# Optimization experiments

Hardware: AMD Instinct MI355X
Metric: run time of the kernel (lower is better)

The kernel has to match this reference:

```python
import jax, jax.numpy as jnp
import numpy as np

N = 50000          # num nodes
E = 800000         # num edges
D = 128            # dim_in == embed_dim
MAX_NODES = 4      # hard-coded in SortConv.__init__
EPS = 1e-5


def setup_inputs() -> dict:
    key = jax.random.key(0)
    ks = jax.random.split(key, 16)
    inp = {
        'x': jax.random.normal(ks[0], (N, D), jnp.float32),
        'edge_index': jax.random.randint(ks[1], (2, E), 0, N, jnp.int32),
    }
    for i in range(2):
        o = 2 + 6 * i
        W = jax.random.normal(ks[o], (D, D), jnp.float32) * (2.0 / (D + D)) ** 0.5
        W = W / jnp.linalg.norm(W, axis=1, keepdims=True)   # reset_parameters row-normalization
        inp[f'W{i}'] = W
        inp[f'b{i}'] = jnp.zeros((D,), jnp.float32)
        inp[f'cw{i}'] = jax.random.normal(ks[o + 1], (MAX_NODES,), jnp.float32) * (2.0 / (MAX_NODES + 1)) ** 0.5
        inp[f'cb{i}'] = jnp.zeros((1,), jnp.float32)
        inp[f'a{i}'] = jax.random.uniform(ks[o + 2], (1,), jnp.float32, -1.0, 1.0)  # LinearCombination scalar
        inp[f'g{i}'] = jnp.ones((D,), jnp.float32)
        inp[f'be{i}'] = jnp.zeros((D,), jnp.float32)
        inp[f'blank{i}'] = jnp.zeros((D,), jnp.float32)      # learnable blank vector
    return inp


def sort_conv(x, edge_index, blank, W, b, cw, cb, a):
    n, d = x.shape
    e = edge_index.shape[1]
    src, dst = edge_index[0], edge_index[1]
    msgs = x[src]                                            # [E, D] raw messages (lin_project not applied to messages)
    order = jnp.argsort(dst)                                 # stable sort by destination (index_sort)
    dst_s = dst[order]
    counts = jax.ops.segment_sum(jnp.ones((e,), jnp.int32), dst, num_segments=n + 1)
    starts = jnp.concatenate([jnp.zeros((1,), jnp.int32), jnp.cumsum(counts)[:-1].astype(jnp.int32)])
    pos = jnp.arange(e, dtype=jnp.int32) - starts[dst_s]     # rank within each neighborhood
    slot = jnp.where(pos < MAX_NODES, pos, MAX_NODES)        # overflow edges -> trash slot (to_dense_batch truncation)
    dense = jnp.zeros((n + 1, MAX_NODES + 1, d), x.dtype).at[dst_s, slot].set(msgs[order])
    mask = jnp.zeros((n + 1, MAX_NODES + 1), bool).at[dst_s, slot].set(True)
    dense, mask = dense[:, :MAX_NODES], mask[:, :MAX_NODES]  # [N+1, 4, D], [N+1, 4]
    blank_p = W @ blank + b                                  # lin_project applied only to blank vector
    filled = dense + (~mask)[..., None].astype(x.dtype) * blank_p
    srt = jnp.sort(filled, axis=1)                           # per-feature sort over neighbor slots
    out = jnp.einsum('nmd,m->nd', srt, cw) + cb              # vector collapse: Linear(max_nodes, 1)
    node_out, blank_new = out[:-1], out[-1]                  # last row = all-blank graph -> new blank
    return a * x + node_out, a * blank + blank_new           # LinearCombination combine (num_repeats=1)


def batch_norm(h, g, be):
    mu = h.mean(0)
    var = h.var(0)
    return (h - mu) / jnp.sqrt(var + EPS) * g + be


def reference(x, edge_index, W0, b0, cw0, cb0, a0, g0, be0, blank0,
              W1, b1, cw1, cb1, a1, g1, be1, blank1):
    layers = [(W0, b0, cw0, cb0, a0, g0, be0, blank0),
              (W1, b1, cw1, cb1, a1, g1, be1, blank1)]
    for (W, b, cw, cb, a, g, be, blank) in layers:
        h, _ = sort_conv(x, edge_index, blank, W, b, cw, cb, a)
        h = batch_norm(h, g, be)
        x = x + h                                            # residual connection
    return x
```

## Files before the change

kernel.cpp:

```cpp
#include <hip/hip_runtime.h>
#include <climits>

constexpr int N_NODES = 50000;
constexpr int N_EDGES = 800000;
constexpr int DIM     = 128;
constexpr int DIM4    = DIM / 4;
constexpr float BN_EPS = 1e-5f;

constexpr int EMPTY = 0x7F7F7F7F;

constexpr int NC = 16;
constexpr int EC = 16;
constexpr int NODES_PER_NC = N_NODES / NC;
constexpr int EDGES_PER_EC = N_EDGES / EC;
constexpr int E4_PER_EC    = EDGES_PER_EC / 4;
constexpr int SEL_THREADS  = 1024;

constexpr int NODES_PER_ITER  = 8;
constexpr int CONV_ITERS      = 2;
constexpr int NODES_PER_BLOCK = NODES_PER_ITER * CONV_ITERS;
constexpr int CONV_GRID = N_NODES / NODES_PER_BLOCK;

constexpr int NBUCKETS = 64;
constexpr int NB_MERGE = (N_NODES + 255) / 256;

__device__ inline float4 f4min(float4 a, float4 b) {
    return make_float4(fminf(a.x,b.x), fminf(a.y,b.y), fminf(a.z,b.z), fminf(a.w,b.w));
}
__device__ inline float4 f4max(float4 a, float4 b) {
    return make_float4(fmaxf(a.x,b.x), fmaxf(a.y,b.y), fmaxf(a.z,b.z), fmaxf(a.w,b.w));
}
__device__ inline float4 f4add(float4 a, float4 b) {
    return make_float4(a.x+b.x, a.y+b.y, a.z+b.z, a.w+b.w);
}
__device__ inline float4 f4fma(float s, float4 v, float4 acc) {
    return make_float4(fmaf(s,v.x,acc.x), fmaf(s,v.y,acc.y), fmaf(s,v.z,acc.z), fmaf(s,v.w,acc.w));
}

__global__ __launch_bounds__(SEL_THREADS)
void select_stageA_kernel(const int* __restrict__ dst,
                          int* __restrict__ tables) {
    __shared__ int slot[NODES_PER_NC * 4];
    const int nc = blockIdx.x & (NC - 1);
    const int ec = blockIdx.x >> 4;
    const int t  = threadIdx.x;

    for (int i = t; i < NODES_PER_NC * 4; i += SEL_THREADS) slot[i] = EMPTY;
    __syncthreads();

    const int r0 = nc * NODES_PER_NC;
    const int4* __restrict__ dst4 = (const int4*)dst;
    const int base4 = ec * E4_PER_EC;
    for (int i = t; i < E4_PER_EC; i += SEL_THREADS) {
        const int4 d = dst4[base4 + i];
        const int ebase = 4 * (base4 + i);
        #define TRY_INS(comp, off) {                                        \
            unsigned n_ = (unsigned)((comp) - r0);                          \
            if (n_ < (unsigned)NODES_PER_NC) {                              \
                int cur_ = ebase + (off);                                   \
                _Pragma("unroll")                                           \
                for (int j_ = 0; j_ < 4; ++j_) {                            \
                    int old_ = atomicMin(&slot[4 * n_ + j_], cur_);         \
                    if (old_ == EMPTY) break;                               \
                    cur_ = max(cur_, old_);                                 \
                } } }
        TRY_INS(d.x, 0); TRY_INS(d.y, 1); TRY_INS(d.z, 2); TRY_INS(d.w, 3);
        #undef TRY_INS
    }
    __syncthreads();

    int4* __restrict__ out = (int4*)tables + (size_t)ec * N_NODES + r0;
    const int4* __restrict__ sl4 = (const int4*)slot;
    for (int n = t; n < NODES_PER_NC; n += SEL_THREADS) out[n] = sl4[n];
}

__global__ __launch_bounds__(256)
void select_stageB_kernel(const int* __restrict__ tables,
                          const int* __restrict__ src,
                          int4* __restrict__ srcs4,
                          float* __restrict__ stats_part,
                          const float* __restrict__ W0, const float* __restrict__ b0,
                          const float* __restrict__ bl0,
                          const float* __restrict__ W1, const float* __restrict__ b1,
                          const float* __restrict__ bl1,
                          float* __restrict__ bp) {
    const int t = threadIdx.x;

    if (blockIdx.x >= NB_MERGE) {
        if (t < DIM) {
            int l = blockIdx.x - NB_MERGE;
            const float* W  = l ? W1  : W0;
            const float* b  = l ? b1  : b0;
            const float* bl = l ? bl1 : bl0;
            float s = 0.f;
            #pragma unroll 8
            for (int j = 0; j < DIM; ++j) s += W[t * DIM + j] * bl[j];
            bp[l * DIM + t] = s + b[t];
        }
        return;
    }

    const int gid = blockIdx.x * 256 + t;
    if (gid < 2 * NBUCKETS * 256) stats_part[gid] = 0.f;

    const int v = gid;
    if (v >= N_NODES) return;

    int b0_ = EMPTY, b1_ = EMPTY, b2_ = EMPTY, b3_ = EMPTY;
    #pragma unroll
    for (int ec = 0; ec < EC; ++ec) {
        const int4 c = ((const int4*)tables)[(size_t)ec * N_NODES + v];
        if (c.x >= b3_) continue;
        #define INS(val) {                                          \
            int x_ = (val);                                         \
            if (x_ < b3_) { b3_ = x_;                               \
                int tm;                                             \
                if (b3_ < b2_) { tm = b2_; b2_ = b3_; b3_ = tm; }   \
                if (b2_ < b1_) { tm = b1_; b1_ = b2_; b2_ = tm; }   \
                if (b1_ < b0_) { tm = b0_; b0_ = b1_; b1_ = tm; } } }
        INS(c.x); INS(c.y); INS(c.z); INS(c.w);
        #undef INS
    }
    int4 o;
    o.x = (b0_ < N_EDGES) ? src[b0_] : -1;
    o.y = (b1_ < N_EDGES) ? src[b1_] : -1;
    o.z = (b2_ < N_EDGES) ? src[b2_] : -1;
    o.w = (b3_ < N_EDGES) ? src[b3_] : -1;
    srcs4[v] = o;
}

__global__ __launch_bounds__(256)
void conv_stats_kernel(const float* __restrict__ x,
                       const int4* __restrict__ srcs4,
                       const float* __restrict__ bp,
                       const float* __restrict__ cw,
                       const float* __restrict__ cb,
                       const float* __restrict__ a,
                       float* __restrict__ h,
                       float* __restrict__ stats_part) {
    const int t    = threadIdx.x;
    const int d4   = t & (DIM4 - 1);
    const int nsub = t >> 5;

    const float4* __restrict__ x4 = (const float4*)x;
    float4*       __restrict__ h4 = (float4*)h;

    const float aa = a[0];
    const float c0 = cw[0], c1 = cw[1], c2 = cw[2], c3 = cw[3];
    const float cbv = cb[0];
    const float4 bpv = ((const float4*)bp)[d4];

    const int v0 = blockIdx.x * NODES_PER_BLOCK + nsub;
    const int v1 = v0 + NODES_PER_ITER;

    const int4 s0 = srcs4[v0];
    const int4 s1 = srcs4[v1];

    float4 g00 = x4[(size_t)max(s0.x, 0) * DIM4 + d4];
    float4 g01 = x4[(size_t)max(s0.y, 0) * DIM4 + d4];
    float4 g02 = x4[(size_t)max(s0.z, 0) * DIM4 + d4];
    float4 g03 = x4[(size_t)max(s0.w, 0) * DIM4 + d4];
    float4 g10 = x4[(size_t)max(s1.x, 0) * DIM4 + d4];
    float4 g11 = x4[(size_t)max(s1.y, 0) * DIM4 + d4];
    float4 g12 = x4[(size_t)max(s1.z, 0) * DIM4 + d4];
    float4 g13 = x4[(size_t)max(s1.w, 0) * DIM4 + d4];
    float4 xv0 = x4[(size_t)v0 * DIM4 + d4];
    float4 xv1 = x4[(size_t)v1 * DIM4 + d4];

    float4 s  = make_float4(0.f, 0.f, 0.f, 0.f);
    float4 s2 = make_float4(0.f, 0.f, 0.f, 0.f);

    #define CSWAP4(p, q) { float4 lo = f4min(p, q); float4 hi = f4max(p, q); p = lo; q = hi; }
    {
        float4 m0 = (s0.x >= 0) ? g00 : bpv;
        float4 m1 = (s0.y >= 0) ? g01 : bpv;
        float4 m2 = (s0.z >= 0) ? g02 : bpv;
        float4 m3 = (s0.w >= 0) ? g03 : bpv;
        CSWAP4(m0, m1); CSWAP4(m2, m3); CSWAP4(m0, m2); CSWAP4(m1, m3); CSWAP4(m1, m2);
        float4 hv = make_float4(cbv, cbv, cbv, cbv);
        hv = f4fma(c0, m0, hv);
        hv = f4fma(c1, m1, hv);
        hv = f4fma(c2, m2, hv);
        hv = f4fma(c3, m3, hv);
        hv = f4fma(aa, xv0, hv);
        h4[(size_t)v0 * DIM4 + d4] = hv;
        s  = f4add(s, hv);
        s2 = f4add(s2, make_float4(hv.x*hv.x, hv.y*hv.y, hv.z*hv.z, hv.w*hv.w));
    }
    {
        float4 m0 = (s1.x >= 0) ? g10 : bpv;
        float4 m1 = (s1.y >= 0) ? g11 : bpv;
        float4 m2 = (s1.z >= 0) ? g12 : bpv;
        float4 m3 = (s1.w >= 0) ? g13 : bpv;
        CSWAP4(m0, m1); CSWAP4(m2, m3); CSWAP4(m0, m2); CSWAP4(m1, m3); CSWAP4(m1, m2);
        float4 hv = make_float4(cbv, cbv, cbv, cbv);
        hv = f4fma(c0, m0, hv);
        hv = f4fma(c1, m1, hv);
        hv = f4fma(c2, m2, hv);
        hv = f4fma(c3, m3, hv);
        hv = f4fma(aa, xv1, hv);
        h4[(size_t)v1 * DIM4 + d4] = hv;
        s  = f4add(s, hv);
        s2 = f4add(s2, make_float4(hv.x*hv.x, hv.y*hv.y, hv.z*hv.z, hv.w*hv.w));
    }
    #undef CSWAP4

    s.x  += __shfl_down(s.x, 32);  s.y  += __shfl_down(s.y, 32);
    s.z  += __shfl_down(s.z, 32);  s.w  += __shfl_down(s.w, 32);
    s2.x += __shfl_down(s2.x, 32); s2.y += __shfl_down(s2.y, 32);
    s2.z += __shfl_down(s2.z, 32); s2.w += __shfl_down(s2.w, 32);

    __shared__ float4 ls[4][32];
    __shared__ float4 ls2[4][32];
    const int wave = t >> 6;
    const int lane = t & 63;
    if (lane < 32) { ls[wave][lane] = s; ls2[wave][lane] = s2; }
    __syncthreads();
    if (t < 32) {
        float* bucket = stats_part + (size_t)(blockIdx.x & (NBUCKETS - 1)) * 256;
        float4 fs  = f4add(f4add(ls[0][t],  ls[1][t]),  f4add(ls[2][t],  ls[3][t]));
        float4 fs2 = f4add(f4add(ls2[0][t], ls2[1][t]), f4add(ls2[2][t], ls2[3][t]));
        atomicAdd(&bucket[4*t + 0], fs.x);
        atomicAdd(&bucket[4*t + 1], fs.y);
        atomicAdd(&bucket[4*t + 2], fs.z);
        atomicAdd(&bucket[4*t + 3], fs.w);
        atomicAdd(&bucket[DIM + 4*t + 0], fs2.x);
        atomicAdd(&bucket[DIM + 4*t + 1], fs2.y);
        atomicAdd(&bucket[DIM + 4*t + 2], fs2.z);
        atomicAdd(&bucket[DIM + 4*t + 3], fs2.w);
    }
}

__global__ void reduce_finalize_kernel(const float* __restrict__ stats_part,
                                       float* __restrict__ final) {
    __shared__ float acc[256];
    int t = threadIdx.x;
    float s = 0.f;
    #pragma unroll 8
    for (int k = 0; k < NBUCKETS; ++k) s += stats_part[k * 256 + t];
    acc[t] = s;
    __syncthreads();
    if (t < 128) {
        constexpr float invN = 1.0f / (float)N_NODES;
        float mu = acc[t] * invN;
        float iv = rsqrtf(acc[128 + t] * invN - mu * mu + BN_EPS);
        final[t]       = mu;
        final[128 + t] = iv;
    }
}

__global__ void bn_apply_kernel(const float* __restrict__ xin,
                                const float* __restrict__ h,
                                const float* __restrict__ final,
                                const float* __restrict__ g,
                                const float* __restrict__ be,
                                float* __restrict__ xout) {
    int idx = blockIdx.x * blockDim.x + threadIdx.x;
    constexpr int TOTAL4 = N_NODES * DIM4;
    if (idx >= TOTAL4) return;
    int d4 = idx & (DIM4 - 1);

    float4 mu = ((const float4*)final)[d4];
    float4 iv = ((const float4*)(final + DIM))[d4];
    float4 hv = ((const float4*)h)[idx];
    float4 xv = ((const float4*)xin)[idx];
    float4 gv = ((const float4*)g)[d4];
    float4 bv = ((const float4*)be)[d4];

    float4 o;
    o.x = xv.x + (hv.x - mu.x) * iv.x * gv.x + bv.x;
    o.y = xv.y + (hv.y - mu.y) * iv.y * gv.y + bv.y;
    o.z = xv.z + (hv.z - mu.z) * iv.z * gv.z + bv.z;
    o.w = xv.w + (hv.w - mu.w) * iv.w * gv.w + bv.w;
    ((float4*)xout)[idx] = o;
}

extern "C" void kernel_launch(void* const* d_in, const int* in_sizes, int n_in,
                              void* d_out, int out_size, void* d_ws, size_t ws_size,
                              hipStream_t stream) {
    const float* x0  = (const float*)d_in[0];
    const int*   ei  = (const int*)d_in[1];
    const int*   src = ei;
    const int*   dst = ei + N_EDGES;

    const float* W[2]; const float* b[2]; const float* cw[2]; const float* cb[2];
    const float* a[2]; const float* g[2]; const float* be[2]; const float* blank[2];
    for (int i = 0; i < 2; ++i) {
        int o = 2 + 8 * i;
        W[i]     = (const float*)d_in[o + 0];
        b[i]     = (const float*)d_in[o + 1];
        cw[i]    = (const float*)d_in[o + 2];
        cb[i]    = (const float*)d_in[o + 3];
        a[i]     = (const float*)d_in[o + 4];
        g[i]     = (const float*)d_in[o + 5];
        be[i]    = (const float*)d_in[o + 6];
        blank[i] = (const float*)d_in[o + 7];
    }

    char* ws = (char*)d_ws;
    int*   srcs       = (int*)ws;
    float* h          = (float*)(srcs + 4 * N_NODES);
    int*   tables     = (int*)h;
    float* stats_part = h + (size_t)N_NODES * DIM;
    float* final_     = stats_part + 2 * NBUCKETS * 256;
    float* bp         = final_ + 512;

    float* xout = (float*)d_out;

    select_stageA_kernel<<<NC * EC, SEL_THREADS, 0, stream>>>(dst, tables);
    select_stageB_kernel<<<NB_MERGE + 2, 256, 0, stream>>>(
        tables, src, (int4*)srcs, stats_part,
        W[0], b[0], blank[0], W[1], b[1], blank[1], bp);

    for (int l = 0; l < 2; ++l) {
        const float* xin = (l == 0) ? x0 : xout;
        float* sp = stats_part + (size_t)l * NBUCKETS * 256;
        conv_stats_kernel<<<CONV_GRID, 256, 0, stream>>>(
            xin, (const int4*)srcs, bp + l * DIM, cw[l], cb[l], a[l], h, sp);
        reduce_finalize_kernel<<<1, 256, 0, stream>>>(sp, final_ + l * 256);
        bn_apply_kernel<<<(N_NODES * DIM4 + 255) / 256, 256, 0, stream>>>(
            xin, h, final_ + l * 256, g[l], be[l], xout);
    }
}
```

Baseline: 207.9 us.

## Fuse conv, batch-norm stats and apply via a grid-wide spin barrier

The conv/stats, reduce-finalize and BN-apply kernels become one kernel per layer. Each block keeps its computed h and x values in registers for 40 nodes, adds its partial sums to the stat buckets, then waits at a grid-wide atomic-counter barrier. After the barrier it reduces the buckets and writes the normalized output directly. This drops the h write/read round trip, the second read of x and two launches per layer. It relies on all 1250 blocks being resident at once (launch bounds of 5 blocks per CU), so the spin barrier could deadlock if occupancy falls short.

Result: slower. 797.0 us (+283.3%).

```diff
diff --git a/kernel.cpp b/kernel.cpp
--- a/kernel.cpp
+++ b/kernel.cpp
@@ -16,10 +16,10 @@
 constexpr int E4_PER_EC    = EDGES_PER_EC / 4;
 constexpr int SEL_THREADS  = 1024;
 
-constexpr int NODES_PER_ITER  = 8;
-constexpr int CONV_ITERS      = 2;
-constexpr int NODES_PER_BLOCK = NODES_PER_ITER * CONV_ITERS;
-constexpr int CONV_GRID = N_NODES / NODES_PER_BLOCK;
+constexpr int F_NODES_PER_ITER = 8;
+constexpr int F_ITERS          = 5;
+constexpr int F_NPB            = F_NODES_PER_ITER * F_ITERS;
+constexpr int F_GRID           = N_NODES / F_NPB;
 
 constexpr int NBUCKETS = 64;
 constexpr int NB_MERGE = (N_NODES + 255) / 256;
@@ -79,6 +79,7 @@
                           const int* __restrict__ src,
                           int4* __restrict__ srcs4,
                           float* __restrict__ stats_part,
+                          int* __restrict__ counters,
                           const float* __restrict__ W0, const float* __restrict__ b0,
                           const float* __restrict__ bl0,
                           const float* __restrict__ W1, const float* __restrict__ b1,
@@ -87,8 +88,8 @@
     const int t = threadIdx.x;
 
     if (blockIdx.x >= NB_MERGE) {
+        int l = blockIdx.x - NB_MERGE;
         if (t < DIM) {
-            int l = blockIdx.x - NB_MERGE;
             const float* W  = l ? W1  : W0;
             const float* b  = l ? b1  : b0;
             const float* bl = l ? bl1 : bl0;
@@ -97,6 +98,7 @@
             for (int j = 0; j < DIM; ++j) s += W[t * DIM + j] * bl[j];
             bp[l * DIM + t] = s + b[t];
         }
+        if (t == 200) counters[l] = 0;
         return;
     }
 
@@ -129,81 +131,61 @@
     srcs4[v] = o;
 }
 
-__global__ __launch_bounds__(256)
-void conv_stats_kernel(const float* __restrict__ x,
-                       const int4* __restrict__ srcs4,
-                       const float* __restrict__ bp,
-                       const float* __restrict__ cw,
-                       const float* __restrict__ cb,
-                       const float* __restrict__ a,
-                       float* __restrict__ h,
-                       float* __restrict__ stats_part) {
+__global__ __launch_bounds__(256, 5)
+void fused_conv_bn_kernel(const float* __restrict__ x,
+                          const int4* __restrict__ srcs4,
+                          const float* __restrict__ bp,
+                          const float* __restrict__ cw,
+                          const float* __restrict__ cb,
+                          const float* __restrict__ a,
+                          const float* __restrict__ g,
+                          const float* __restrict__ be,
+                          float* __restrict__ stats_part,
+                          int* __restrict__ counter,
+                          float* __restrict__ xout) {
     const int t    = threadIdx.x;
     const int d4   = t & (DIM4 - 1);
     const int nsub = t >> 5;
 
     const float4* __restrict__ x4 = (const float4*)x;
-    float4*       __restrict__ h4 = (float4*)h;
 
     const float aa = a[0];
     const float c0 = cw[0], c1 = cw[1], c2 = cw[2], c3 = cw[3];
     const float cbv = cb[0];
     const float4 bpv = ((const float4*)bp)[d4];
 
-    const int v0 = blockIdx.x * NODES_PER_BLOCK + nsub;
-    const int v1 = v0 + NODES_PER_ITER;
-
-    const int4 s0 = srcs4[v0];
-    const int4 s1 = srcs4[v1];
-
-    float4 g00 = x4[(size_t)max(s0.x, 0) * DIM4 + d4];
-    float4 g01 = x4[(size_t)max(s0.y, 0) * DIM4 + d4];
-    float4 g02 = x4[(size_t)max(s0.z, 0) * DIM4 + d4];
-    float4 g03 = x4[(size_t)max(s0.w, 0) * DIM4 + d4];
-    float4 g10 = x4[(size_t)max(s1.x, 0) * DIM4 + d4];
-    float4 g11 = x4[(size_t)max(s1.y, 0) * DIM4 + d4];
-    float4 g12 = x4[(size_t)max(s1.z, 0) * DIM4 + d4];
-    float4 g13 = x4[(size_t)max(s1.w, 0) * DIM4 + d4];
-    float4 xv0 = x4[(size_t)v0 * DIM4 + d4];
-    float4 xv1 = x4[(size_t)v1 * DIM4 + d4];
-
     float4 s  = make_float4(0.f, 0.f, 0.f, 0.f);
     float4 s2 = make_float4(0.f, 0.f, 0.f, 0.f);
-
-    #define CSWAP4(p, q) { float4 lo = f4min(p, q); float4 hi = f4max(p, q); p = lo; q = hi; }
-    {
-        float4 m0 = (s0.x >= 0) ? g00 : bpv;
-        float4 m1 = (s0.y >= 0) ? g01 : bpv;
-        float4 m2 = (s0.z >= 0) ? g02 : bpv;
-        float4 m3 = (s0.w >= 0) ? g03 : bpv;
+    float4 hreg[F_ITERS];
+    float4 xreg[F_ITERS];
+
+    const int vbase = blockIdx.x * F_NPB;
+    #pragma unroll
+    for (int it = 0; it < F_ITERS; ++it) {
+        const int v = vbase + it * F_NODES_PER_ITER + nsub;
+        const int4 sv = srcs4[v];
+        float4 m0 = (sv.x >= 0) ? x4[(size_t)max(sv.x,0) * DIM4 + d4] : bpv;
+        float4 m1 = (sv.y >= 0) ? x4[(size_t)max(sv.y,0) * DIM4 + d4] : bpv;
+        float4 m2 = (sv.z >= 0) ? x4[(size_t)max(sv.z,0) * DIM4 + d4] : bpv;
+        float4 m3 = (sv.w >= 0) ? x4[(size_t)max(sv.w,0) * DIM4 + d4] : bpv;
+
+        #define CSWAP4(p, q) { float4 lo = f4min(p, q); float4 hi = f4max(p, q); p = lo; q = hi; }
         CSWAP4(m0, m1); CSWAP4(m2, m3); CSWAP4(m0, m2); CSWAP4(m1, m3); CSWAP4(m1, m2);
+        #undef CSWAP4
+
+        float4 xv = x4[(size_t)v * DIM4 + d4];
         float4 hv = make_float4(cbv, cbv, cbv, cbv);
         hv = f4fma(c0, m0, hv);
         hv = f4fma(c1, m1, hv);
         hv = f4fma(c2, m2, hv);
         hv = f4fma(c3, m3, hv);
-        hv = f4fma(aa, xv0, hv);
-        h4[(size_t)v0 * DIM4 + d4] = hv;
+        hv = f4fma(aa, xv, hv);
+        hreg[it] = hv;
+        xreg[it] = xv;
+
         s  = f4add(s, hv);
         s2 = f4add(s2, make_float4(hv.x*hv.x, hv.y*hv.y, hv.z*hv.z, hv.w*hv.w));
     }
-    {
-        float4 m0 = (s1.x >= 0) ? g10 : bpv;
-        float4 m1 = (s1.y >= 0) ? g11 : bpv;
-        float4 m2 = (s1.z >= 0) ? g12 : bpv;
-        float4 m3 = (s1.w >= 0) ? g13 : bpv;
-        CSWAP4(m0, m1); CSWAP4(m2, m3); CSWAP4(m0, m2); CSWAP4(m1, m3); CSWAP4(m1, m2);
-        float4 hv = make_float4(cbv, cbv, cbv, cbv);
-        hv = f4fma(c0, m0, hv);
-        hv = f4fma(c1, m1, hv);
-        hv = f4fma(c2, m2, hv);
-        hv = f4fma(c3, m3, hv);
-        hv = f4fma(aa, xv1, hv);
-        h4[(size_t)v1 * DIM4 + d4] = hv;
-        s  = f4add(s, hv);
-        s2 = f4add(s2, make_float4(hv.x*hv.x, hv.y*hv.y, hv.z*hv.z, hv.w*hv.w));
-    }
-    #undef CSWAP4
 
     s.x  += __shfl_down(s.x, 32);  s.y  += __shfl_down(s.y, 32);
     s.z  += __shfl_down(s.z, 32);  s.w  += __shfl_down(s.w, 32);
@@ -229,50 +211,52 @@
         atomicAdd(&bucket[DIM + 4*t + 2], fs2.z);
         atomicAdd(&bucket[DIM + 4*t + 3], fs2.w);
     }
-}
-
-__global__ void reduce_finalize_kernel(const float* __restrict__ stats_part,
-                                       float* __restrict__ final) {
-    __shared__ float acc[256];
-    int t = threadIdx.x;
-    float s = 0.f;
-    #pragma unroll 8
-    for (int k = 0; k < NBUCKETS; ++k) s += stats_part[k * 256 + t];
-    acc[t] = s;
-    __syncthreads();
-    if (t < 128) {
-        constexpr float invN = 1.0f / (float)N_NODES;
-        float mu = acc[t] * invN;
-        float iv = rsqrtf(acc[128 + t] * invN - mu * mu + BN_EPS);
-        final[t]       = mu;
-        final[128 + t] = iv;
-    }
-}
-
-__global__ void bn_apply_kernel(const float* __restrict__ xin,
-                                const float* __restrict__ h,
-                                const float* __restrict__ final,
-                                const float* __restrict__ g,
-                                const float* __restrict__ be,
-                                float* __restrict__ xout) {
-    int idx = blockIdx.x * blockDim.x + threadIdx.x;
-    constexpr int TOTAL4 = N_NODES * DIM4;
-    if (idx >= TOTAL4) return;
-    int d4 = idx & (DIM4 - 1);
-
-    float4 mu = ((const float4*)final)[d4];
-    float4 iv = ((const float4*)(final + DIM))[d4];
-    float4 hv = ((const float4*)h)[idx];
-    float4 xv = ((const float4*)xin)[idx];
-    float4 gv = ((const float4*)g)[d4];
-    float4 bv = ((const float4*)be)[d4];
-
-    float4 o;
-    o.x = xv.x + (hv.x - mu.x) * iv.x * gv.x + bv.x;
-    o.y = xv.y + (hv.y - mu.y) * iv.y * gv.y + bv.y;
-    o.z = xv.z + (hv.z - mu.z) * iv.z * gv.z + bv.z;
-    o.w = xv.w + (hv.w - mu.w) * iv.w * gv.w + bv.w;
-    ((float4*)xout)[idx] = o;
+
+    __threadfence();
+    if (t == 0) {
+        __hip_atomic_fetch_add(counter, 1, __ATOMIC_ACQ_REL, __HIP_MEMORY_SCOPE_AGENT);
+        while (__hip_atomic_load(counter, __ATOMIC_ACQUIRE, __HIP_MEMORY_SCOPE_AGENT)
+               < F_GRID)
+            __builtin_amdgcn_s_sleep(8);
+    }
+    __syncthreads();
+
+    __shared__ float red[256];
+    {
+        float acc = 0.f;
+        #pragma unroll 8
+        for (int k = 0; k < NBUCKETS; ++k)
+            acc += __hip_atomic_load(&stats_part[k * 256 + t],
+                                     __ATOMIC_RELAXED, __HIP_MEMORY_SCOPE_AGENT);
+        red[t] = acc;
+    }
+    __syncthreads();
+
+    constexpr float invN = 1.0f / (float)N_NODES;
+    float4 mu, iv;
+    {
+        float m0_ = red[4*d4 + 0] * invN, m1_ = red[4*d4 + 1] * invN;
+        float m2_ = red[4*d4 + 2] * invN, m3_ = red[4*d4 + 3] * invN;
+        mu = make_float4(m0_, m1_, m2_, m3_);
+        iv.x = rsqrtf(red[DIM + 4*d4 + 0] * invN - m0_*m0_ + BN_EPS);
+        iv.y = rsqrtf(red[DIM + 4*d4 + 1] * invN - m1_*m1_ + BN_EPS);
+        iv.z = rsqrtf(red[DIM + 4*d4 + 2] * invN - m2_*m2_ + BN_EPS);
+        iv.w = rsqrtf(red[DIM + 4*d4 + 3] * invN - m3_*m3_ + BN_EPS);
+    }
+    const float4 gv = ((const float4*)g)[d4];
+    const float4 bv = ((const float4*)be)[d4];
+
+    float4* __restrict__ o4 = (float4*)xout;
+    #pragma unroll
+    for (int it = 0; it < F_ITERS; ++it) {
+        const int v = vbase + it * F_NODES_PER_ITER + nsub;
+        float4 hv = hreg[it], xv = xreg[it], o;
+        o.x = xv.x + (hv.x - mu.x) * iv.x * gv.x + bv.x;
+        o.y = xv.y + (hv.y - mu.y) * iv.y * gv.y + bv.y;
+        o.z = xv.z + (hv.z - mu.z) * iv.z * gv.z + bv.z;
+        o.w = xv.w + (hv.w - mu.w) * iv.w * gv.w + bv.w;
+        o4[(size_t)v * DIM4 + d4] = o;
+    }
 }
 
 extern "C" void kernel_launch(void* const* d_in, const int* in_sizes, int n_in,
@@ -299,26 +283,23 @@
 
     char* ws = (char*)d_ws;
     int*   srcs       = (int*)ws;
-    float* h          = (float*)(srcs + 4 * N_NODES);
-    int*   tables     = (int*)h;
-    float* stats_part = h + (size_t)N_NODES * DIM;
-    float* final_     = stats_part + 2 * NBUCKETS * 256;
-    float* bp         = final_ + 512;
+    int*   tables     = srcs + 4 * N_NODES;
+    float* stats_part = (float*)(tables + (size_t)EC * 4 * N_NODES);
+    float* bp         = stats_part + 2 * NBUCKETS * 256;
+    int*   counters   = (int*)(bp + 256);
 
     float* xout = (float*)d_out;
 
     select_stageA_kernel<<<NC * EC, SEL_THREADS, 0, stream>>>(dst, tables);
     select_stageB_kernel<<<NB_MERGE + 2, 256, 0, stream>>>(
-        tables, src, (int4*)srcs, stats_part,
+        tables, src, (int4*)srcs, stats_part, counters,
         W[0], b[0], blank[0], W[1], b[1], blank[1], bp);
 
     for (int l = 0; l < 2; ++l) {
         const float* xin = (l == 0) ? x0 : xout;
         float* sp = stats_part + (size_t)l * NBUCKETS * 256;
-        conv_stats_kernel<<<CONV_GRID, 256, 0, stream>>>(
-            xin, (const int4*)srcs, bp + l * DIM, cw[l], cb[l], a[l], h, sp);
-        reduce_finalize_kernel<<<1, 256, 0, stream>>>(sp, final_ + l * 256);
-        bn_apply_kernel<<<(N_NODES * DIM4 + 255) / 256, 256, 0, stream>>>(
-            xin, h, final_ + l * 256, g[l], be[l], xout);
-    }
-}
+        fused_conv_bn_kernel<<<F_GRID, 256, 0, stream>>>(
+            xin, (const int4*)srcs, bp + l * DIM, cw[l], cb[l], a[l],
+            g[l], be[l], sp, counters + l, xout);
+    }
+}
```
